# Performance work log

Hardware: AMD Instinct MI355X
Metric: run time of the kernel (lower is better)

## Reference

```python
import jax, jax.numpy as jnp
import numpy as np

N = 1048576
NUM_FREQS = 4
NUM_DIM = 3
NUM_QUANTS = 80
NUM_FEATS = 4
MIN_LOG2_FREQ = 1.0
MAX_LOG2_FREQ = 6.0
NUM_LINES = 2 * NUM_FREQS * NUM_DIM  # sin/cos x freq x axis = 24
LATENT = NUM_LINES * NUM_FEATS       # 96


def setup_inputs() -> dict:
    key = jax.random.key(0)
    ks = jax.random.split(key, 8)
    positions = jax.random.uniform(ks[0], (N, NUM_DIM), jnp.float32, -1.0, 1.0)
    d = jax.random.normal(ks[1], (N, NUM_DIM), jnp.float32)
    directions = d / jnp.linalg.norm(d, axis=-1, keepdims=True)
    grid = jax.random.normal(ks[2], (NUM_LINES, NUM_QUANTS, NUM_FEATS), jnp.float32) * 0.1
    w_geom1 = jax.random.normal(ks[3], (LATENT, 64), jnp.float32) * (1.0 / np.sqrt(LATENT))
    w_geom2 = jax.random.normal(ks[4], (64, 16), jnp.float32) * (1.0 / 8.0)
    w_color1 = jax.random.normal(ks[5], (31, 64), jnp.float32) * (1.0 / np.sqrt(31.0))
    w_color2 = jax.random.normal(ks[6], (64, 64), jnp.float32) * (1.0 / 8.0)
    w_color3 = jax.random.normal(ks[7], (64, 3), jnp.float32) * (1.0 / 8.0)
    return {"positions": positions, "directions": directions, "grid": grid,
            "w_geom1": w_geom1, "w_geom2": w_geom2,
            "w_color1": w_color1, "w_color2": w_color2, "w_color3": w_color3}


@jax.custom_vjp
def trunc_exp(x):
    return jnp.exp(x)

def _te_fwd(x):
    return jnp.exp(x), x

def _te_bwd(x, g):
    return (g * jnp.exp(jnp.clip(x, -15.0, 15.0)),)

trunc_exp.defvjp(_te_fwd, _te_bwd)


def spherical_harmonics16(d):
    # degree-4 (l=0..3) real SH basis, 16 components, torch-ngp coefficients
    x, y, z = d[:, 0], d[:, 1], d[:, 2]
    xx, yy, zz = x * x, y * y, z * z
    xy, yz, xz = x * y, y * z, x * z
    return jnp.stack([
        jnp.full_like(x, 0.28209479177387814),
        -0.48860251190291987 * y,
        0.48860251190291987 * z,
        -0.48860251190291987 * x,
        1.0925484305920792 * xy,
        -1.0925484305920792 * yz,
        0.94617469575755997 * zz - 0.31539156525251999,
        -1.0925484305920792 * xz,
        0.54627421529603959 * (xx - yy),
        -0.59004358992664352 * y * (3.0 * xx - yy),
        2.8906114426405538 * xy * z,
        -0.45704579946446572 * y * (4.0 * zz - xx - yy),
        0.37317633259011546 * z * (2.0 * zz - 3.0 * xx - 3.0 * yy),
        -0.45704579946446572 * x * (4.0 * zz - xx - yy),
        1.4453057213202769 * z * (xx - yy),
        -0.59004358992664352 * x * (xx - 3.0 * yy),
    ], axis=-1)  # [N, 16]


def qff1_encode(positions, grid):
    # frequencies 2^linspace(min,max,F)
    freqs = 2.0 ** jnp.linspace(MIN_LOG2_FREQ, MAX_LOG2_FREQ, NUM_FREQS).astype(jnp.float32)
    # phase: [N, D, F]
    p = positions[:, :, None] * freqs[None, None, :]
    coords = jnp.concatenate([jnp.sin(p), jnp.cos(p)], axis=-1)  # [N, D, 2F]
    coords = coords.transpose(0, 2, 1).reshape(positions.shape[0], NUM_LINES)  # [N, L]
    # map [-1,1] -> continuous grid coord and linearly interpolate 1D lines
    u = (coords + 1.0) * 0.5 * (NUM_QUANTS - 1)
    i0 = jnp.clip(jnp.floor(u).astype(jnp.int32), 0, NUM_QUANTS - 2)
    w = (u - i0.astype(u.dtype))[..., None]  # [N, L, 1]
    lidx = jnp.arange(NUM_LINES)[None, :]
    g0 = grid[lidx, i0]      # [N, L, C]
    g1 = grid[lidx, i0 + 1]  # [N, L, C]
    feat = g0 * (1.0 - w) + g1 * w
    return feat.reshape(positions.shape[0], LATENT)


def _forward(positions, directions, grid, w_geom1, w_geom2, w_color1, w_color2, w_color3):
    enc = qff1_encode(positions, grid)                    # [N, 96]
    h = jax.nn.relu(enc @ w_geom1)                        # [N, 64]
    f = h @ w_geom2                                       # [N, 16]
    raw_sigma, feature = f[:, :1], f[:, 1:]
    density = trunc_exp(raw_sigma - 1.0)                  # [N, 1]
    sh = spherical_harmonics16(directions)                # [N, 16]
    hc = jnp.concatenate([sh, feature], axis=-1)          # [N, 31]
    hc = jax.nn.relu(hc @ w_color1)
    hc = jax.nn.relu(hc @ w_color2)
    rgb = jax.nn.sigmoid(hc @ w_color3)                   # [N, 3]
    return rgb, density


def reference(positions, directions, grid, w_geom1, w_geom2, w_color1, w_color2, w_color3):
    return _forward(positions, directions, grid, w_geom1, w_geom2, w_color1, w_color2, w_color3)
```

## Files before the change

### kernel.cpp

```cpp
#include <hip/hip_runtime.h>
#include <stdint.h>


typedef _Float16 half8  __attribute__((ext_vector_type(8)));
typedef _Float16 h2     __attribute__((ext_vector_type(2)));
typedef float    f32x16 __attribute__((ext_vector_type(16)));

union FragU { uint32_t u[4]; uint4 q; half8 h; };
union H2U   { uint32_t u; h2 h; };

static __device__ __forceinline__ h2 bch2(uint32_t v) { H2U x; x.u = v; return x.h; }
static __device__ __forceinline__ uint32_t bcu(h2 v)  { H2U x; x.h = v; return x.u; }

static __device__ __forceinline__ h2 cvtpk(float lo, float hi) {
  return __builtin_bit_cast(h2, __builtin_amdgcn_cvt_pkrtz(lo, hi));
}
static __device__ __forceinline__ uint32_t pkrtz(float lo, float hi) {
  return bcu(cvtpk(lo, hi));
}
static __device__ __forceinline__ void plswap_u(uint32_t &a, uint32_t &b) {
  asm("v_permlane32_swap_b32 %0, %1" : "+v"(a), "+v"(b));
}
static __device__ __forceinline__ void plswap_f(float &a, float &b) {
  asm("v_permlane32_swap_b32 %0, %1" : "+v"(a), "+v"(b));
}
static __device__ __forceinline__ half8 mk_frag(uint32_t a, uint32_t b, uint32_t c, uint32_t d) {
  FragU f; f.u[0] = a; f.u[1] = b; f.u[2] = c; f.u[3] = d; return f.h;
}
static __device__ __forceinline__ uint32_t maxz(uint32_t v) {
  h2 h = bch2(v); h = __builtin_elementwise_max(h, (h2)(_Float16)0.0f); return bcu(h);
}
static __device__ __forceinline__ unsigned short f16b(float v) {
  _Float16 h = (_Float16)v; return __builtin_bit_cast(unsigned short, h);
}

#define MFMA(A, B, C) __builtin_amdgcn_mfma_f32_32x32x16_f16((A), (B), (C), 0, 0, 0)

#define W1OFF   0
#define W2OFF   13312
#define WC1OFF  17920
#define WC2OFF  23040
#define WC3OFF  32256
#define GROFF   36864
#define LDSZ    52224
#define WBYTES  36864

static __device__ __forceinline__ half8 ldw(const unsigned char* s, int row, int off) {
  FragU f; f.q = *(const uint4*)(s + row + off); return f.h;
}

template<int BASE, bool RELU>
static __device__ __forceinline__ half8 packB(const f32x16& a) {
  uint32_t x = pkrtz(a[BASE + 0], a[BASE + 1]);
  uint32_t z = pkrtz(a[BASE + 2], a[BASE + 3]);
  uint32_t y = pkrtz(a[BASE + 4], a[BASE + 5]);
  uint32_t w = pkrtz(a[BASE + 6], a[BASE + 7]);
  if (RELU) { x = maxz(x); z = maxz(z); y = maxz(y); w = maxz(w); }
  plswap_u(x, y);
  plswap_u(z, w);
  return mk_frag(x, z, y, w);
}

struct Pre {
  float m[6];
  int   gbs[12];
  int   a13, a9, a5;
};

template<int J>
static __device__ __forceinline__ void gather(const Pre& pre, float q0, float q1, float q2,
                                              const unsigned char* lds,
                                              uint32_t& w01, uint32_t& w23) {
  constexpr int jm = J % 6;
  constexpr int DIMP[6] = {0, 1, 1, 2, 2, 0};
  float q = (DIMP[jm] == 0) ? q0 : ((DIMP[jm] == 1) ? q1 : q2);
  float r = fmaf(q, pre.m[jm], (J < 6) ? 0.0f : 0.25f);
  r = __builtin_amdgcn_fractf(r);
  float s = __builtin_amdgcn_sinf(r);
  float u = fmaf(s, 39.5f, 39.5f);
  int i0 = (int)u;
  i0 = i0 < 0 ? 0 : (i0 > 78 ? 78 : i0);
  float w = u - (float)i0;
  const unsigned char* base = lds + pre.gbs[J] + (i0 << 2);
  uint32_t a0 = *(const uint32_t*)(base);
  uint32_t b0 = *(const uint32_t*)(base + 4);
  uint32_t a1 = *(const uint32_t*)(base + 320);
  uint32_t b1 = *(const uint32_t*)(base + 324);
  h2 wh = cvtpk(w, w);
  h2 f01 = __builtin_elementwise_fma(bch2(b0) - bch2(a0), wh, bch2(a0));
  h2 f23 = __builtin_elementwise_fma(bch2(b1) - bch2(a1), wh, bch2(a1));
  w01 = bcu(f01);
  w23 = bcu(f23);
}

template<int T>
static __device__ __forceinline__ half8 enc2(const Pre& pre, float q0, float q1, float q2,
                                             const unsigned char* lds) {
  uint32_t a, b, c, d;
  gather<2 * T + 0>(pre, q0, q1, q2, lds, a, b);
  gather<2 * T + 1>(pre, q0, q1, q2, lds, c, d);
  return mk_frag(a, b, c, d);
}

__global__ __launch_bounds__(512, 4)
void qff_fwd(const float* __restrict__ pos, const float* __restrict__ dir,
             const float* __restrict__ grid,
             const float* __restrict__ w1, const float* __restrict__ w2,
             const float* __restrict__ wc1, const float* __restrict__ wc2,
             const float* __restrict__ wc3,
             float* __restrict__ out, int Npts) {
  __shared__ __align__(16) unsigned char smem[LDSZ];
  const int tid = threadIdx.x;

  for (int i = tid; i < WBYTES / 4; i += 512) ((uint32_t*)smem)[i] = 0;
  __syncthreads();
  for (int i = tid; i < 6144; i += 512)
    *(unsigned short*)(smem + W1OFF  + (i & 63) * 208 + (i >> 6) * 2) = f16b(w1[i]);
  for (int i = tid; i < 1024; i += 512)
    *(unsigned short*)(smem + W2OFF  + (i & 15) * 144 + (i >> 4) * 2) = f16b(w2[i]);
  for (int i = tid; i < 1984; i += 512)
    *(unsigned short*)(smem + WC1OFF + (i & 63) * 80  + (i >> 6) * 2) = f16b(wc1[i]);
  for (int i = tid; i < 4096; i += 512)
    *(unsigned short*)(smem + WC2OFF + (i & 63) * 144 + (i >> 6) * 2) = f16b(wc2[i]);
  for (int i = tid; i < 192; i += 512)
    *(unsigned short*)(smem + WC3OFF + (i % 3) * 144 + (i / 3) * 2) = f16b(wc3[i]);
  for (int i = tid; i < 1920; i += 512) {
    float4 v = ((const float4*)grid)[i];
    int line = i / 80, q = i - line * 80;
    uint32_t* dst = (uint32_t*)(smem + GROFF + line * 640 + q * 4);
    dst[0]  = (((uint32_t)f16b(v.y)) << 16) | f16b(v.x);
    dst[80] = (((uint32_t)f16b(v.w)) << 16) | f16b(v.z);
  }
  __syncthreads();

  const int lane = tid & 63;
  const int wid  = tid >> 6;
  const int g    = lane >> 5;
  const int o    = lane & 31;

  constexpr float IV = 0.15915494309189535f;
  constexpr float F0 = 2.0f, F1 = 6.349604207872798f, F2 = 20.158736798317971f, F3 = 64.0f;
  const float M0c[6] = {F0*IV, F0*IV, F1*IV, F1*IV, F2*IV, F3*IV};
  const float M1c[6] = {F0*IV, F1*IV, F2*IV, F2*IV, F3*IV, F3*IV};
  const int   LNS0[6] = {0, 1, 4, 5, 8, 9};
  const int   LNS1[6] = {2, 3, 6, 7, 10, 11};
  Pre pre;
#pragma unroll
  for (int j = 0; j < 6; ++j) {
    pre.m[j] = g ? M1c[j] : M0c[j];
    int ln = g ? LNS1[j] : LNS0[j];
    pre.gbs[j]     = GROFF + ln * 640;
    pre.gbs[j + 6] = GROFF + (ln + 12) * 640;
  }
  pre.a13 = o * 208 + g * 16;
  pre.a9  = o * 144 + g * 16;
  pre.a5  = o * 80  + g * 16;

  const f32x16 Z = {0,0,0,0, 0,0,0,0, 0,0,0,0, 0,0,0,0};
  const int ntile = Npts >> 8;
  int tb = blockIdx.x;
  if (tb >= ntile) return;

  int p = (tb << 8) + (wid << 5) + o;
  float px = pos[3*p+0], py = pos[3*p+1], pz = pos[3*p+2];
  float dx = dir[3*p+0], dy = dir[3*p+1], dz = dir[3*p+2];

  for (; tb < ntile; tb += gridDim.x) {
    int tbn = tb + gridDim.x;
    int pn  = ((tbn < ntile ? tbn : ntile - 1) << 8) + (wid << 5) + o;
    float npx = pos[3*pn+0], npy = pos[3*pn+1], npz = pos[3*pn+2];
    float ndx = dir[3*pn+0], ndy = dir[3*pn+1], ndz = dir[3*pn+2];

    float q0 = g ? pz : px;
    float q1 = g ? px : py;
    float q2 = g ? py : pz;

    f32x16 acc0 = Z, acc1 = Z;
#define L1STEP(T) { half8 bf = enc2<T>(pre, q0, q1, q2, smem); \
                    acc0 = MFMA(ldw(smem, pre.a13, W1OFF + T*32), bf, acc0); \
                    acc1 = MFMA(ldw(smem, pre.a13, W1OFF + 6656 + T*32), bf, acc1); }
    L1STEP(0) L1STEP(1) L1STEP(2) L1STEP(3) L1STEP(4) L1STEP(5)
#undef L1STEP

    half8 hb0 = packB<0, true>(acc0), hb1 = packB<8, true>(acc0);
    half8 hb2 = packB<0, true>(acc1), hb3 = packB<8, true>(acc1);

    f32x16 acc2 = Z;
    acc2 = MFMA(ldw(smem, pre.a9, W2OFF +  0), hb0, acc2);
    acc2 = MFMA(ldw(smem, pre.a9, W2OFF + 32), hb1, acc2);
    acc2 = MFMA(ldw(smem, pre.a9, W2OFF + 64), hb2, acc2);
    acc2 = MFMA(ldw(smem, pre.a9, W2OFF + 96), hb3, acc2);
    float sigma = __expf(acc2[0] - 1.0f);

    float xx = dx*dx, yy = dy*dy, zz = dz*dz;
    float xy = dx*dy, yz = dy*dz, xz = dx*dz;
    float s0, s1, s2, s3, s4, s5, s6, s7;
    if (g == 0) {
      s0 = 0.28209479177387814f;
      s1 = -0.48860251190291987f * dy;
      s2 =  0.48860251190291987f * dz;
      s3 = -0.48860251190291987f * dx;
      s4 =  1.0925484305920792f * xy;
      s5 = -1.0925484305920792f * yz;
      s6 =  0.94617469575756f * zz - 0.31539156525252f;
      s7 = -1.0925484305920792f * xz;
    } else {
      s0 =  0.5462742152960396f * (xx - yy);
      s1 = -0.5900435899266435f * dy * (3.0f * xx - yy);
      s2 =  2.890611442640554f * xy * dz;
      s3 = -0.4570457994644657f * dy * (4.0f * zz - xx - yy);
      s4 =  0.37317633259011546f * dz * (2.0f * zz - 3.0f * xx - 3.0f * yy);
      s5 = -0.4570457994644657f * dx * (4.0f * zz - xx - yy);
      s6 =  1.445305721320277f * dz * (xx - yy);
      s7 = -0.5900435899266435f * dx * (xx - 3.0f * yy);
    }
    half8 shB = mk_frag(pkrtz(s0, s1), pkrtz(s2, s3), pkrtz(s4, s5), pkrtz(s6, s7));

    uint32_t e0 = pkrtz(acc2[1], acc2[2]);
    uint32_t e2 = pkrtz(acc2[5], acc2[6]);
    plswap_u(e0, e2);
    float a3 = acc2[3], b7 = acc2[7];
    plswap_f(a3, b7);
    float cc0 = acc2[0], d4 = acc2[4];
    plswap_f(cc0, d4);
    uint32_t e1 = pkrtz(a3, d4);
    uint32_t e3 = pkrtz(b7, acc2[4]);
    half8 featB = mk_frag(e0, e1, e2, e3);

    f32x16 acc3a = Z, acc3b = Z;
    acc3a = MFMA(ldw(smem, pre.a5, WC1OFF +  0), shB,   acc3a);
    acc3a = MFMA(ldw(smem, pre.a5, WC1OFF + 32), featB, acc3a);
    acc3b = MFMA(ldw(smem, pre.a5, WC1OFF + 2560 +  0), shB,   acc3b);
    acc3b = MFMA(ldw(smem, pre.a5, WC1OFF + 2560 + 32), featB, acc3b);

    half8 g2b0 = packB<0, true>(acc3a), g2b1 = packB<8, true>(acc3a);
    half8 g2b2 = packB<0, true>(acc3b), g2b3 = packB<8, true>(acc3b);

    f32x16 acc4a = Z, acc4b = Z;
    acc4a = MFMA(ldw(smem, pre.a9, WC2OFF +  0), g2b0, acc4a);
    acc4a = MFMA(ldw(smem, pre.a9, WC2OFF + 32), g2b1, acc4a);
    acc4a = MFMA(ldw(smem, pre.a9, WC2OFF + 64), g2b2, acc4a);
    acc4a = MFMA(ldw(smem, pre.a9, WC2OFF + 96), g2b3, acc4a);
    acc4b = MFMA(ldw(smem, pre.a9, WC2OFF + 4608 +  0), g2b0, acc4b);
    acc4b = MFMA(ldw(smem, pre.a9, WC2OFF + 4608 + 32), g2b1, acc4b);
    acc4b = MFMA(ldw(smem, pre.a9, WC2OFF + 4608 + 64), g2b2, acc4b);
    acc4b = MFMA(ldw(smem, pre.a9, WC2OFF + 4608 + 96), g2b3, acc4b);

    half8 g3b0 = packB<0, true>(acc4a), g3b1 = packB<8, true>(acc4a);
    half8 g3b2 = packB<0, true>(acc4b), g3b3 = packB<8, true>(acc4b);

    f32x16 acc5 = Z;
    acc5 = MFMA(ldw(smem, pre.a9, WC3OFF +  0), g3b0, acc5);
    acc5 = MFMA(ldw(smem, pre.a9, WC3OFF + 32), g3b1, acc5);
    acc5 = MFMA(ldw(smem, pre.a9, WC3OFF + 64), g3b2, acc5);
    acc5 = MFMA(ldw(smem, pre.a9, WC3OFF + 96), g3b3, acc5);

    if (lane < 32) {
      float rr = __builtin_amdgcn_rcpf(1.0f + __expf(-acc5[0]));
      float gg = __builtin_amdgcn_rcpf(1.0f + __expf(-acc5[1]));
      float bb = __builtin_amdgcn_rcpf(1.0f + __expf(-acc5[2]));
      out[3 * p + 0] = rr;
      out[3 * p + 1] = gg;
      out[3 * p + 2] = bb;
      out[3 * Npts + p] = sigma;
    }

    p = pn;
    px = npx; py = npy; pz = npz;
    dx = ndx; dy = ndy; dz = ndz;
  }
}

extern "C" void kernel_launch(void* const* d_in, const int* in_sizes, int n_in,
                              void* d_out, int out_size, void* d_ws, size_t ws_size,
                              hipStream_t stream) {
  const float* pos  = (const float*)d_in[0];
  const float* dirs = (const float*)d_in[1];
  const float* grid = (const float*)d_in[2];
  const float* w1   = (const float*)d_in[3];
  const float* w2   = (const float*)d_in[4];
  const float* wc1  = (const float*)d_in[5];
  const float* wc2  = (const float*)d_in[6];
  const float* wc3  = (const float*)d_in[7];
  float* out = (float*)d_out;
  const int Npts = in_sizes[0] / 3;

  qff_fwd<<<dim3(512), dim3(512), 0, stream>>>(pos, dirs, grid, w1, w2, wc1, wc2, wc3,
                                               out, Npts);
}
```

Measured before the change: 51.77 us.

## Pin all MLP weight fragments in registers and halve occupancy target

```diff
diff --git a/kernel.cpp b/kernel.cpp
--- a/kernel.cpp
+++ b/kernel.cpp
@@ -45,8 +45,10 @@
 #define LDSZ    52224
 #define WBYTES  36864
 
-static __device__ __forceinline__ half8 ldw(const unsigned char* s, int row, int off) {
-  FragU f; f.q = *(const uint4*)(s + row + off); return f.h;
+static __device__ __forceinline__ half8 ldwp(const unsigned char* s, int row, int off) {
+  FragU f; f.q = *(const uint4*)(s + row + off);
+  asm volatile("" : "+v"(f.u[0]), "+v"(f.u[1]), "+v"(f.u[2]), "+v"(f.u[3]));
+  return f.h;
 }
 
 template<int BASE, bool RELU>
@@ -61,27 +63,24 @@
   return mk_frag(x, z, y, w);
 }
 
-struct Pre {
-  float m[6];
-  int   gbs[12];
-  int   a13, a9, a5;
-};
-
 template<int J>
-static __device__ __forceinline__ void gather(const Pre& pre, float q0, float q1, float q2,
+static __device__ __forceinline__ void gather(const float* m, int gbase,
+                                              float q0, float q1, float q2,
                                               const unsigned char* lds,
                                               uint32_t& w01, uint32_t& w23) {
   constexpr int jm = J % 6;
   constexpr int DIMP[6] = {0, 1, 1, 2, 2, 0};
+  constexpr int LNS0[6] = {0, 1, 4, 5, 8, 9};
+  constexpr int GOFFJ = (LNS0[jm] + (J < 6 ? 0 : 12)) * 640;
   float q = (DIMP[jm] == 0) ? q0 : ((DIMP[jm] == 1) ? q1 : q2);
-  float r = fmaf(q, pre.m[jm], (J < 6) ? 0.0f : 0.25f);
+  float r = fmaf(q, m[jm], (J < 6) ? 0.0f : 0.25f);
   r = __builtin_amdgcn_fractf(r);
   float s = __builtin_amdgcn_sinf(r);
   float u = fmaf(s, 39.5f, 39.5f);
   int i0 = (int)u;
   i0 = i0 < 0 ? 0 : (i0 > 78 ? 78 : i0);
   float w = u - (float)i0;
-  const unsigned char* base = lds + pre.gbs[J] + (i0 << 2);
+  const unsigned char* base = lds + gbase + GOFFJ + (i0 << 2);
   uint32_t a0 = *(const uint32_t*)(base);
   uint32_t b0 = *(const uint32_t*)(base + 4);
   uint32_t a1 = *(const uint32_t*)(base + 320);
@@ -94,15 +93,16 @@
 }
 
 template<int T>
-static __device__ __forceinline__ half8 enc2(const Pre& pre, float q0, float q1, float q2,
+static __device__ __forceinline__ half8 enc2(const float* m, int gbase,
+                                             float q0, float q1, float q2,
                                              const unsigned char* lds) {
   uint32_t a, b, c, d;
-  gather<2 * T + 0>(pre, q0, q1, q2, lds, a, b);
-  gather<2 * T + 1>(pre, q0, q1, q2, lds, c, d);
+  gather<2 * T + 0>(m, gbase, q0, q1, q2, lds, a, b);
+  gather<2 * T + 1>(m, gbase, q0, q1, q2, lds, c, d);
   return mk_frag(a, b, c, d);
 }
 
-__global__ __launch_bounds__(512, 4)
+__global__ __launch_bounds__(512, 2)
 void qff_fwd(const float* __restrict__ pos, const float* __restrict__ dir,
              const float* __restrict__ grid,
              const float* __restrict__ w1, const float* __restrict__ w2,
@@ -138,23 +138,36 @@
   const int g    = lane >> 5;
   const int o    = lane & 31;
 
+  const int a13 = o * 208 + g * 16;
+  const int a9  = o * 144 + g * 16;
+  const int a5  = o * 80  + g * 16;
+  half8 w1f[2][6], w2f[4], c1f[2][2], c2f[2][4], c3f[4];
+#pragma unroll
+  for (int t = 0; t < 6; ++t) {
+    w1f[0][t] = ldwp(smem, a13, W1OFF + t * 32);
+    w1f[1][t] = ldwp(smem, a13, W1OFF + 6656 + t * 32);
+  }
+#pragma unroll
+  for (int t = 0; t < 4; ++t) {
+    w2f[t]    = ldwp(smem, a9, W2OFF + t * 32);
+    c2f[0][t] = ldwp(smem, a9, WC2OFF + t * 32);
+    c2f[1][t] = ldwp(smem, a9, WC2OFF + 4608 + t * 32);
+    c3f[t]    = ldwp(smem, a9, WC3OFF + t * 32);
+  }
+#pragma unroll
+  for (int t = 0; t < 2; ++t) {
+    c1f[0][t] = ldwp(smem, a5, WC1OFF + t * 32);
+    c1f[1][t] = ldwp(smem, a5, WC1OFF + 2560 + t * 32);
+  }
+
   constexpr float IV = 0.15915494309189535f;
   constexpr float F0 = 2.0f, F1 = 6.349604207872798f, F2 = 20.158736798317971f, F3 = 64.0f;
   const float M0c[6] = {F0*IV, F0*IV, F1*IV, F1*IV, F2*IV, F3*IV};
   const float M1c[6] = {F0*IV, F1*IV, F2*IV, F2*IV, F3*IV, F3*IV};
-  const int   LNS0[6] = {0, 1, 4, 5, 8, 9};
-  const int   LNS1[6] = {2, 3, 6, 7, 10, 11};
-  Pre pre;
+  float m[6];
 #pragma unroll
-  for (int j = 0; j < 6; ++j) {
-    pre.m[j] = g ? M1c[j] : M0c[j];
-    int ln = g ? LNS1[j] : LNS0[j];
-    pre.gbs[j]     = GROFF + ln * 640;
-    pre.gbs[j + 6] = GROFF + (ln + 12) * 640;
-  }
-  pre.a13 = o * 208 + g * 16;
-  pre.a9  = o * 144 + g * 16;
-  pre.a5  = o * 80  + g * 16;
+  for (int j = 0; j < 6; ++j) m[j] = g ? M1c[j] : M0c[j];
+  const int gbase = GROFF + g * 1280;
 
   const f32x16 Z = {0,0,0,0, 0,0,0,0, 0,0,0,0, 0,0,0,0};
   const int ntile = Npts >> 8;
@@ -176,9 +189,9 @@
     float q2 = g ? py : pz;
 
     f32x16 acc0 = Z, acc1 = Z;
-#define L1STEP(T) { half8 bf = enc2<T>(pre, q0, q1, q2, smem); \
-                    acc0 = MFMA(ldw(smem, pre.a13, W1OFF + T*32), bf, acc0); \
-                    acc1 = MFMA(ldw(smem, pre.a13, W1OFF + 6656 + T*32), bf, acc1); }
+#define L1STEP(T) { half8 bf = enc2<T>(m, gbase, q0, q1, q2, smem); \
+                    acc0 = MFMA(w1f[0][T], bf, acc0); \
+                    acc1 = MFMA(w1f[1][T], bf, acc1); }
     L1STEP(0) L1STEP(1) L1STEP(2) L1STEP(3) L1STEP(4) L1STEP(5)
 #undef L1STEP
 
@@ -186,10 +199,10 @@
     half8 hb2 = packB<0, true>(acc1), hb3 = packB<8, true>(acc1);
 
     f32x16 acc2 = Z;
-    acc2 = MFMA(ldw(smem, pre.a9, W2OFF +  0), hb0, acc2);
-    acc2 = MFMA(ldw(smem, pre.a9, W2OFF + 32), hb1, acc2);
-    acc2 = MFMA(ldw(smem, pre.a9, W2OFF + 64), hb2, acc2);
-    acc2 = MFMA(ldw(smem, pre.a9, W2OFF + 96), hb3, acc2);
+    acc2 = MFMA(w2f[0], hb0, acc2);
+    acc2 = MFMA(w2f[1], hb1, acc2);
+    acc2 = MFMA(w2f[2], hb2, acc2);
+    acc2 = MFMA(w2f[3], hb3, acc2);
     float sigma = __expf(acc2[0] - 1.0f);
 
     float xx = dx*dx, yy = dy*dy, zz = dz*dz;
@@ -228,32 +241,32 @@
     half8 featB = mk_frag(e0, e1, e2, e3);
 
     f32x16 acc3a = Z, acc3b = Z;
-    acc3a = MFMA(ldw(smem, pre.a5, WC1OFF +  0), shB,   acc3a);
-    acc3a = MFMA(ldw(smem, pre.a5, WC1OFF + 32), featB, acc3a);
-    acc3b = MFMA(ldw(smem, pre.a5, WC1OFF + 2560 +  0), shB,   acc3b);
-    acc3b = MFMA(ldw(smem, pre.a5, WC1OFF + 2560 + 32), featB, acc3b);
+    acc3a = MFMA(c1f[0][0], shB,   acc3a);
+    acc3a = MFMA(c1f[0][1], featB, acc3a);
+    acc3b = MFMA(c1f[1][0], shB,   acc3b);
+    acc3b = MFMA(c1f[1][1], featB, acc3b);
 
     half8 g2b0 = packB<0, true>(acc3a), g2b1 = packB<8, true>(acc3a);
     half8 g2b2 = packB<0, true>(acc3b), g2b3 = packB<8, true>(acc3b);
 
     f32x16 acc4a = Z, acc4b = Z;
-    acc4a = MFMA(ldw(smem, pre.a9, WC2OFF +  0), g2b0, acc4a);
-    acc4a = MFMA(ldw(smem, pre.a9, WC2OFF + 32), g2b1, acc4a);
-    acc4a = MFMA(ldw(smem, pre.a9, WC2OFF + 64), g2b2, acc4a);
-    acc4a = MFMA(ldw(smem, pre.a9, WC2OFF + 96), g2b3, acc4a);
-    acc4b = MFMA(ldw(smem, pre.a9, WC2OFF + 4608 +  0), g2b0, acc4b);
-    acc4b = MFMA(ldw(smem, pre.a9, WC2OFF + 4608 + 32), g2b1, acc4b);
-    acc4b = MFMA(ldw(smem, pre.a9, WC2OFF + 4608 + 64), g2b2, acc4b);
-    acc4b = MFMA(ldw(smem, pre.a9, WC2OFF + 4608 + 96), g2b3, acc4b);
+    acc4a = MFMA(c2f[0][0], g2b0, acc4a);
+    acc4a = MFMA(c2f[0][1], g2b1, acc4a);
+    acc4a = MFMA(c2f[0][2], g2b2, acc4a);
+    acc4a = MFMA(c2f[0][3], g2b3, acc4a);
+    acc4b = MFMA(c2f[1][0], g2b0, acc4b);
+    acc4b = MFMA(c2f[1][1], g2b1, acc4b);
+    acc4b = MFMA(c2f[1][2], g2b2, acc4b);
+    acc4b = MFMA(c2f[1][3], g2b3, acc4b);
 
     half8 g3b0 = packB<0, true>(acc4a), g3b1 = packB<8, true>(acc4a);
     half8 g3b2 = packB<0, true>(acc4b), g3b3 = packB<8, true>(acc4b);
 
     f32x16 acc5 = Z;
-    acc5 = MFMA(ldw(smem, pre.a9, WC3OFF +  0), g3b0, acc5);
-    acc5 = MFMA(ldw(smem, pre.a9, WC3OFF + 32), g3b1, acc5);
-    acc5 = MFMA(ldw(smem, pre.a9, WC3OFF + 64), g3b2, acc5);
-    acc5 = MFMA(ldw(smem, pre.a9, WC3OFF + 96), g3b3, acc5);
+    acc5 = MFMA(c3f[0], g3b0, acc5);
+    acc5 = MFMA(c3f[1], g3b1, acc5);
+    acc5 = MFMA(c3f[2], g3b2, acc5);
+    acc5 = MFMA(c3f[3], g3b3, acc5);
 
     if (lane < 32) {
       float rr = __builtin_amdgcn_rcpf(1.0f + __expf(-acc5[0]));
```

After: 53.44 us. 1.03x slower.
